# Kernel optimization log

Measured on AMD Instinct MI355X. Metric: run time of the kernel, lower is better.

## Reference

```python
import jax, jax.numpy as jnp
import numpy as np

D = 256        # n_unit
H = 2          # n_head
FF = 256       # n_hid
WIN = 99       # N-1 in source: row i attends to cols [i-99, i]
NEG = -1e30    # additive mask value (-inf in torch)
LN_EPS = 1e-5


def _layer_norm(x, w, b):
    mu = jnp.mean(x, axis=-1, keepdims=True)
    var = jnp.mean((x - mu) ** 2, axis=-1, keepdims=True)
    return (x - mu) * jax.lax.rsqrt(var + LN_EPS) * w + b


def _pos_encoding(S, d):
    pos = jnp.arange(S, dtype=jnp.float32)[:, None]                      # [S,1]
    div = jnp.exp(jnp.arange(0, d, 2, dtype=jnp.float32) * (-np.log(10000.0) / d))
    ang = pos * div                                                      # [S,d/2]
    return jnp.stack([jnp.sin(ang), jnp.cos(ang)], axis=-1).reshape(S, d)


def _band_mask(S):
    i = jnp.arange(S)[:, None]
    j = jnp.arange(S)[None, :]
    allowed = (j <= i) & (j >= i - WIN)
    return jnp.where(allowed, 0.0, NEG).astype(jnp.float32)             # [S,S]


def setup_inputs() -> dict:
    key = jax.random.key(0)
    ks = jax.random.split(key, 24)
    B, S, IN = 8, 2000, 256
    s = 0.02
    inp = {
        "src": jax.random.normal(ks[0], (B, S, IN), jnp.float32),
        "input_lengths": jax.random.randint(ks[1], (B,), 1, S + 1).astype(jnp.int64),
        # encoder Linear(in_size, n_unit); torch Linear weight is [out,in]
        "W_enc": jax.random.normal(ks[2], (D, IN), jnp.float32) * s,
        "b_enc": jnp.zeros((D,), jnp.float32),
        # MHA packed qkv projection
        "in_proj_w": jax.random.normal(ks[3], (3 * D, D), jnp.float32) * s,
        "in_proj_b": jnp.zeros((3 * D,), jnp.float32),
        "out_proj_w": jax.random.normal(ks[4], (D, D), jnp.float32) * s,
        "out_proj_b": jnp.zeros((D,), jnp.float32),
        "ln1_w": jnp.ones((D,), jnp.float32),
        "ln1_b": jnp.zeros((D,), jnp.float32),
        # FFN
        "lin1_w": jax.random.normal(ks[5], (FF, D), jnp.float32) * s,
        "lin1_b": jnp.zeros((FF,), jnp.float32),
        "lin2_w": jax.random.normal(ks[6], (D, FF), jnp.float32) * s,
        "lin2_b": jnp.zeros((D,), jnp.float32),
        "ln2_w": jnp.ones((D,), jnp.float32),
        "ln2_b": jnp.zeros((D,), jnp.float32),
        # output head
        "fc1_w": jax.random.normal(ks[7], (D // 4, D), jnp.float32) * s,
        "fc1_b": jnp.zeros((D // 4,), jnp.float32),
        "fc2_w": jax.random.normal(ks[8], (1, D // 4), jnp.float32) * s,
        "fc2_b": jnp.zeros((1,), jnp.float32),
    }
    return inp


def reference(src, input_lengths, W_enc, b_enc, in_proj_w, in_proj_b,
              out_proj_w, out_proj_b, ln1_w, ln1_b, lin1_w, lin1_b,
              lin2_w, lin2_b, ln2_w, ln2_b, fc1_w, fc1_b, fc2_w, fc2_b):
    B, S, _ = src.shape
    hd = D // H
    # input projection + positional encoding (dropout is identity at eval)
    x = src @ W_enc.T + b_enc                                            # [B,S,D]
    x = x + _pos_encoding(S, D)[None]
    # --- TransformerEncoderLayer (post-norm, relu) with banded causal mask ---
    qkv = x @ in_proj_w.T + in_proj_b                                    # [B,S,3D]
    q, k, v = jnp.split(qkv, 3, axis=-1)
    q = q.reshape(B, S, H, hd)
    k = k.reshape(B, S, H, hd)
    v = v.reshape(B, S, H, hd)
    scores = jnp.einsum('bihd,bjhd->bhij', q, k) / np.sqrt(hd)           # [B,H,S,S]
    scores = scores + _band_mask(S)[None, None]
    attn = jax.nn.softmax(scores, axis=-1)
    ctx = jnp.einsum('bhij,bjhd->bihd', attn, v).reshape(B, S, D)
    attn_out = ctx @ out_proj_w.T + out_proj_b
    x = _layer_norm(x + attn_out, ln1_w, ln1_b)
    ff = jax.nn.relu(x @ lin1_w.T + lin1_b) @ lin2_w.T + lin2_b
    x = _layer_norm(x + ff, ln2_w, ln2_b)
    # --- output head (no activation between fc1 and fc2, per source) ---
    out = x @ fc1_w.T + fc1_b                                            # [B,S,D/4]
    logits = out @ fc2_w.T + fc2_b                                       # [B,S,1]
    return logits.reshape(B, -1)                                         # [B,S]
```

## Files before the change

kernel.cpp:

```cpp
#include <hip/hip_runtime.h>
#include <math.h>

#define SLEN 2000
#define BATCH 8
#define MTOK 16000
#define WIN 99

typedef __attribute__((ext_vector_type(8))) short short8;
typedef __attribute__((ext_vector_type(4))) float floatx4;

__device__ __forceinline__ float bf2f(unsigned int h) {
  union { unsigned int u; float f; } w; w.u = h << 16; return w.f;
}
__device__ __forceinline__ unsigned short f2bf(float f) {
  union { float f; unsigned int u; } w; w.f = f;
  return (unsigned short)((w.u + 0x7fffu + ((w.u >> 16) & 1u)) >> 16);
}

typedef const __attribute__((address_space(1))) unsigned int* gas_t;
typedef __attribute__((address_space(3))) unsigned int* las_t;
__device__ __forceinline__ void gload_lds16(const unsigned short* g, unsigned short* l) {
  __builtin_amdgcn_global_load_lds((gas_t)g, (las_t)l, 16, 0, 0);
}

__device__ __forceinline__ void cvt4(const float* __restrict__ in,
                                     unsigned short* __restrict__ out, int i) {
  float4 v = ((const float4*)in)[i];
  ushort4 o;
  o.x = f2bf(v.x); o.y = f2bf(v.y); o.z = f2bf(v.z); o.w = f2bf(v.w);
  ((ushort4*)out)[i] = o;
}

__global__ __launch_bounds__(256) void k_prep(
    const float* __restrict__ wenc,     unsigned short* __restrict__ wencb,
    const float* __restrict__ wqk,      unsigned short* __restrict__ wqkb,
    const float* __restrict__ wout,     unsigned short* __restrict__ woutb,
    const float* __restrict__ wl1,      unsigned short* __restrict__ wl1b,
    const float* __restrict__ wl2,      unsigned short* __restrict__ wl2b,
    float* __restrict__ pe,
    const float* __restrict__ fc1w, const float* __restrict__ fc1b,
    const float* __restrict__ fc2w, const float* __restrict__ fc2b,
    const float* __restrict__ ln2w, const float* __restrict__ ln2b,
    float* __restrict__ hp) {
  __shared__ float red0[4], red1[4];
  const int bx = blockIdx.x, tid = threadIdx.x;
  if (bx < 64)         { cvt4(wenc, wencb, bx * 256 + tid); }
  else if (bx < 256)   { cvt4(wqk,  wqkb,  (bx - 64) * 256 + tid); }
  else if (bx < 320)   { cvt4(wout, woutb, (bx - 256) * 256 + tid); }
  else if (bx < 384)   { cvt4(wl1,  wl1b,  (bx - 320) * 256 + tid); }
  else if (bx < 448)   { cvt4(wl2,  wl2b,  (bx - 384) * 256 + tid); }
  else if (bx < 2448) {
    int idx = (bx - 448) * 256 + tid;
    int s = idx >> 8, d = idx & 255, p2 = d >> 1;
    float dv  = expf((float)p2 * -0.07195578415606394f);
    float ang = (float)s * dv;
    pe[idx] = (d & 1) ? cosf(ang) : sinf(ang);
  } else {
    int k = tid;
    float we = 0.f;
#pragma unroll 8
    for (int o = 0; o < 64; ++o) we += fc2w[o] * fc1w[o * 256 + k];
    float c1 = ln2w[k] * we;
    hp[k] = c1;
    float p0 = ln2b[k] * we;
    if (k < 64) p0 += fc2w[k] * fc1b[k];
    float s0 = p0, s1 = c1;
#pragma unroll
    for (int off = 32; off; off >>= 1) {
      s0 += __shfl_xor(s0, off);
      s1 += __shfl_xor(s1, off);
    }
    int wv = k >> 6;
    if ((k & 63) == 0) { red0[wv] = s0; red1[wv] = s1; }
    __syncthreads();
    if (k == 0) {
      hp[256] = red0[0] + red0[1] + red0[2] + red0[3] + fc2b[0];
      hp[257] = red1[0] + red1[1] + red1[2] + red1[3];
    }
  }
}

#define XPAD 264

__global__ __launch_bounds__(256) void k_pre(
    const float* __restrict__ src,
    const unsigned short* __restrict__ wenc, const float* __restrict__ benc,
    const float* __restrict__ pe,
    const unsigned short* __restrict__ wqk, const float* __restrict__ bqk,
    unsigned short* __restrict__ xb, unsigned short* __restrict__ qkvb) {
  __shared__ __align__(16) unsigned short Xt[64 * XPAD];
  __shared__ __align__(16) unsigned short Achk[64 * 32];
  __shared__ __align__(16) unsigned short Bchk[256 * 32];
  const int tid = threadIdx.x, lane = tid & 63, w = tid >> 6;
  const int m0 = blockIdx.x * 64;
  const int kq = lane >> 4, ml = lane & 15;
  const int myrow = w * 16 + ml;
  const int cq = lane >> 4, cl = lane & 15;

  const int ar = tid >> 2, as = tid & 3;
  const int ac = as ^ ((ar >> 1) & 3);
  const float* asrc = src + (size_t)(m0 + ar) * 256 + ac * 8;

  int brow[4], bsc[4];
#pragma unroll
  for (int i = 0; i < 4; ++i) {
    brow[i] = (w * 4 + i) * 16 + (lane >> 2);
    bsc[i]  = (lane & 3) ^ ((brow[i] >> 1) & 3);
  }

  floatx4 acc[16] = {};
  for (int kt = 0; kt < 256; kt += 32) {
    __syncthreads();
    {
      float4 v0 = *(const float4*)(asrc + kt);
      float4 v1 = *(const float4*)(asrc + kt + 4);
      unsigned short t8[8] = {f2bf(v0.x), f2bf(v0.y), f2bf(v0.z), f2bf(v0.w),
                              f2bf(v1.x), f2bf(v1.y), f2bf(v1.z), f2bf(v1.w)};
      *(uint4*)&Achk[ar * 32 + as * 8] = *(const uint4*)t8;
    }
#pragma unroll
    for (int i = 0; i < 4; ++i)
      gload_lds16(wenc + (size_t)brow[i] * 256 + kt + bsc[i] * 8, &Bchk[(w * 4 + i) * 512]);
    __syncthreads();

    int sa = kq ^ ((myrow >> 1) & 3);
    short8 af = *(const short8*)&Achk[myrow * 32 + sa * 8];
#pragma unroll
    for (int nt = 0; nt < 16; ++nt) {
      int n = nt * 16 + ml;
      int sb = kq ^ ((n >> 1) & 3);
      short8 bf = *(const short8*)&Bchk[n * 32 + sb * 8];
      acc[nt] = __builtin_amdgcn_mfma_f32_16x16x32_bf16(af, bf, acc[nt], 0, 0, 0);
    }
  }
#pragma unroll
  for (int nt = 0; nt < 16; ++nt) {
#pragma unroll
    for (int r = 0; r < 4; ++r) {
      int lrow = w * 16 + cq * 4 + r;
      int row  = m0 + lrow;
      int col  = nt * 16 + cl;
      float v = acc[nt][r] + benc[col] + pe[(size_t)(row % SLEN) * 256 + col];
      unsigned short hv = f2bf(v);
      Xt[lrow * XPAD + col] = hv;
      xb[(size_t)row * 256 + col] = hv;
    }
  }

  for (int p = 0; p < 3; ++p) {
    floatx4 a2[16] = {};
    for (int kt = 0; kt < 256; kt += 32) {
      __syncthreads();
#pragma unroll
      for (int i = 0; i < 4; ++i)
        gload_lds16(wqk + (size_t)(p * 256 + brow[i]) * 256 + kt + bsc[i] * 8,
                    &Bchk[(w * 4 + i) * 512]);
      __syncthreads();
      short8 af = *(const short8*)&Xt[myrow * XPAD + kt + kq * 8];
#pragma unroll
      for (int nt = 0; nt < 16; ++nt) {
        int n = nt * 16 + ml;
        int sb = kq ^ ((n >> 1) & 3);
        short8 bf = *(const short8*)&Bchk[n * 32 + sb * 8];
        a2[nt] = __builtin_amdgcn_mfma_f32_16x16x32_bf16(af, bf, a2[nt], 0, 0, 0);
      }
    }
#pragma unroll
    for (int nt = 0; nt < 16; ++nt) {
#pragma unroll
      for (int r = 0; r < 4; ++r) {
        int row = m0 + w * 16 + cq * 4 + r;
        int cg  = p * 256 + nt * 16 + cl;
        qkvb[(size_t)row * 768 + cg] = f2bf(a2[nt][r] + bqk[cg]);
      }
    }
  }
}

#define KPAD 136
#define VPAD 184
#define PPAD 132
#define UNION 176

__global__ __launch_bounds__(256) void k_attn_mfma(const unsigned short* __restrict__ qkv,
                                                   unsigned short* __restrict__ ctx) {
  __shared__ __align__(16) unsigned short KV[UNION * KPAD];
  __shared__ __align__(16) unsigned short Ps[4][16 * PPAD];
  const int tid  = threadIdx.x;
  const int lane = tid & 63;
  const int w    = tid >> 6;
  const int i0   = blockIdx.x * 64;
  const int b    = blockIdx.y;
  const int h    = blockIdx.z;
  const int jmin_u = i0 - WIN;
  const float scale = 0.08838834764831845f;

  const int qrow = i0 + w * 16 + (lane & 15);
  const unsigned short* qptr =
      qkv + (size_t)(b * SLEN + min(qrow, SLEN - 1)) * 768 + h * 128 + (lane >> 4) * 8;
  short8 qf[4];
#pragma unroll
  for (int kc = 0; kc < 4; ++kc) qf[kc] = *(const short8*)(qptr + kc * 32);

  for (int it = 0; it < 11; ++it) {
    int idx = it * 256 + tid;
    int row = idx >> 4;
    int c8  = idx & 15;
    int j = jmin_u + row;
    uint4 v = make_uint4(0u, 0u, 0u, 0u);
    if (j >= 0 && j < SLEN)
      v = *(const uint4*)(qkv + (size_t)(b * SLEN + j) * 768 + 256 + h * 128 + c8 * 8);
    *(uint4*)&KV[row * KPAD + c8 * 8] = v;
  }
  __syncthreads();

  const int koff = w * 16;
  floatx4 sc[8] = {};
#pragma unroll
  for (int kt = 0; kt < 8; ++kt) {
#pragma unroll
    for (int kc = 0; kc < 4; ++kc) {
      short8 kf = *(const short8*)&KV[(koff + kt * 16 + (lane & 15)) * KPAD
                                      + kc * 32 + (lane >> 4) * 8];
      sc[kt] = __builtin_amdgcn_mfma_f32_16x16x32_bf16(qf[kc], kf, sc[kt], 0, 0, 0);
    }
  }

  const int qme = i0 + w * 16 + (lane >> 4) * 4;
  const int jme = jmin_u + koff + (lane & 15);
  float mx[4] = {-1e30f, -1e30f, -1e30f, -1e30f};
#pragma unroll
  for (int kt = 0; kt < 8; ++kt) {
#pragma unroll
    for (int r = 0; r < 4; ++r) {
      int j = jme + kt * 16, q = qme + r;
      bool ok = (j >= 0) && (j >= q - WIN) && (j <= q);
      float s = ok ? sc[kt][r] : -1e30f;
      sc[kt][r] = s;
      mx[r] = fmaxf(mx[r], s);
    }
  }
#pragma unroll
  for (int r = 0; r < 4; ++r)
#pragma unroll
    for (int off = 8; off; off >>= 1) mx[r] = fmaxf(mx[r], __shfl_xor(mx[r], off, 16));

  float sum[4] = {0.f, 0.f, 0.f, 0.f};
#pragma unroll
  for (int kt = 0; kt < 8; ++kt)
#pragma unroll
    for (int r = 0; r < 4; ++r) {
      float e = __expf((sc[kt][r] - mx[r]) * scale);
      sc[kt][r] = e;
      sum[r] += e;
    }
#pragma unroll
  for (int r = 0; r < 4; ++r)
#pragma unroll
    for (int off = 8; off; off >>= 1) sum[r] += __shfl_xor(sum[r], off, 16);
  float rinv[4];
#pragma unroll
  for (int r = 0; r < 4; ++r) rinv[r] = 1.f / sum[r];

  unsigned short* pw = &Ps[w][0];
#pragma unroll
  for (int kt = 0; kt < 8; ++kt)
#pragma unroll
    for (int r = 0; r < 4; ++r)
      pw[((lane >> 4) * 4 + r) * PPAD + kt * 16 + (lane & 15)] = f2bf(sc[kt][r]);
  __syncthreads();

  for (int it = 0; it < 12; ++it) {
    int idx = it * 256 + tid;
    int grp = idx >> 6;
    int key = (grp >> 4) * 64 + (idx & 63);
    int c8  = grp & 15;
    if (key < UNION) {
      int j = jmin_u + key;
      uint4 v = make_uint4(0u, 0u, 0u, 0u);
      if (j >= 0 && j < SLEN)
        v = *(const uint4*)(qkv + (size_t)(b * SLEN + j) * 768 + 512 + h * 128 + c8 * 8);
      unsigned short e[8];
      *(uint4*)e = v;
      int d0 = c8 * 8;
#pragma unroll
      for (int i = 0; i < 8; ++i) KV[(d0 + i) * VPAD + key] = e[i];
    }
  }
  __syncthreads();

  floatx4 ov[8] = {};
#pragma unroll
  for (int kc = 0; kc < 4; ++kc) {
    short8 pf = *(const short8*)&pw[(lane & 15) * PPAD + kc * 32 + (lane >> 4) * 8];
#pragma unroll
    for (int dt = 0; dt < 8; ++dt) {
      short8 vf = *(const short8*)&KV[(dt * 16 + (lane & 15)) * VPAD
                                      + koff + kc * 32 + (lane >> 4) * 8];
      ov[dt] = __builtin_amdgcn_mfma_f32_16x16x32_bf16(pf, vf, ov[dt], 0, 0, 0);
    }
  }

#pragma unroll
  for (int dt = 0; dt < 8; ++dt)
#pragma unroll
    for (int r = 0; r < 4; ++r) {
      int q = qme + r;
      if (q < SLEN)
        ctx[(size_t)(b * SLEN + q) * 256 + h * 128 + dt * 16 + (lane & 15)] =
            f2bf(ov[dt][r] * rinv[r]);
    }
}

__global__ __launch_bounds__(256) void k_post(
    const unsigned short* __restrict__ ctx,
    const unsigned short* __restrict__ wout, const float* __restrict__ bout,
    const unsigned short* __restrict__ xb,
    const float* __restrict__ ln1w, const float* __restrict__ ln1b,
    const unsigned short* __restrict__ w1, const float* __restrict__ b1,
    const unsigned short* __restrict__ w2, const float* __restrict__ b2,
    const float* __restrict__ hp, float* __restrict__ out) {
  __shared__ __align__(16) unsigned short X1[64 * XPAD];
  __shared__ __align__(16) unsigned short Achk[64 * 32];
  __shared__ __align__(16) unsigned short Bchk[256 * 32];
  __shared__ float lnp[512];
  __shared__ float c1s[256];
  const int tid = threadIdx.x, lane = tid & 63, w = tid >> 6;
  const int m0 = blockIdx.x * 64;
  const int kq = lane >> 4, ml = lane & 15;
  const int myrow = w * 16 + ml;
  const int cq = lane >> 4, cl = lane & 15;

  lnp[tid] = ln1w[tid];
  lnp[256 + tid] = ln1b[tid];
  c1s[tid] = hp[tid];
  const float c0 = hp[256], sc1 = hp[257];

  int brow[4], bsc[4];
#pragma unroll
  for (int i = 0; i < 4; ++i) {
    brow[i] = (w * 4 + i) * 16 + (lane >> 2);
    bsc[i]  = (lane & 3) ^ ((brow[i] >> 1) & 3);
  }
  const int arow = w * 16 + (lane >> 2);
  const int asc  = (lane & 3) ^ ((arow >> 1) & 3);
  const unsigned short* actx = ctx + (size_t)(m0 + arow) * 256 + asc * 8;

  floatx4 acc[16] = {};
  for (int kt = 0; kt < 256; kt += 32) {
    __syncthreads();
    gload_lds16(actx + kt, &Achk[w * 512]);
#pragma unroll
    for (int i = 0; i < 4; ++i)
      gload_lds16(wout + (size_t)brow[i] * 256 + kt + bsc[i] * 8, &Bchk[(w * 4 + i) * 512]);
    __syncthreads();
    int sa = kq ^ ((myrow >> 1) & 3);
    short8 af = *(const short8*)&Achk[myrow * 32 + sa * 8];
#pragma unroll
    for (int nt = 0; nt < 16; ++nt) {
      int n = nt * 16 + ml;
      int sb = kq ^ ((n >> 1) & 3);
      short8 bf = *(const short8*)&Bchk[n * 32 + sb * 8];
      acc[nt] = __builtin_amdgcn_mfma_f32_16x16x32_bf16(af, bf, acc[nt], 0, 0, 0);
    }
  }
  float s_[4] = {0.f, 0.f, 0.f, 0.f}, q_[4] = {0.f, 0.f, 0.f, 0.f};
#pragma unroll
  for (int nt = 0; nt < 16; ++nt) {
#pragma unroll
    for (int r = 0; r < 4; ++r) {
      int row = m0 + w * 16 + cq * 4 + r;
      int col = nt * 16 + cl;
      float v = acc[nt][r] + bout[col] + bf2f(xb[(size_t)row * 256 + col]);
      acc[nt][r] = v;
      s_[r] += v;
      q_[r] += v * v;
    }
  }
#pragma unroll
  for (int r = 0; r < 4; ++r)
#pragma unroll
    for (int off = 8; off; off >>= 1) {
      s_[r] += __shfl_xor(s_[r], off, 16);
      q_[r] += __shfl_xor(q_[r], off, 16);
    }
  floatx4 x1sav[16];
#pragma unroll
  for (int r = 0; r < 4; ++r) {
    float mu  = s_[r] * (1.f / 256.f);
    float var = q_[r] * (1.f / 256.f) - mu * mu;
    float rr  = rsqrtf(var + 1e-5f);
    int lrow  = w * 16 + cq * 4 + r;
#pragma unroll
    for (int nt = 0; nt < 16; ++nt) {
      int col = nt * 16 + cl;
      float x1 = (acc[nt][r] - mu) * rr * lnp[col] + lnp[256 + col];
      x1sav[nt][r] = x1;
      X1[lrow * XPAD + col] = f2bf(x1);
    }
  }

#pragma unroll
  for (int nt = 0; nt < 16; ++nt) acc[nt] = (floatx4){0.f, 0.f, 0.f, 0.f};
  for (int kt = 0; kt < 256; kt += 32) {
    __syncthreads();
#pragma unroll
    for (int i = 0; i < 4; ++i)
      gload_lds16(w1 + (size_t)brow[i] * 256 + kt + bsc[i] * 8, &Bchk[(w * 4 + i) * 512]);
    __syncthreads();
    short8 af = *(const short8*)&X1[myrow * XPAD + kt + kq * 8];
#pragma unroll
    for (int nt = 0; nt < 16; ++nt) {
      int n = nt * 16 + ml;
      int sb = kq ^ ((n >> 1) & 3);
      short8 bf = *(const short8*)&Bchk[n * 32 + sb * 8];
      acc[nt] = __builtin_amdgcn_mfma_f32_16x16x32_bf16(af, bf, acc[nt], 0, 0, 0);
    }
  }
  __syncthreads();
#pragma unroll
  for (int nt = 0; nt < 16; ++nt) {
#pragma unroll
    for (int r = 0; r < 4; ++r) {
      int lrow = w * 16 + cq * 4 + r;
      int col  = nt * 16 + cl;
      X1[lrow * XPAD + col] = f2bf(fmaxf(acc[nt][r] + b1[col], 0.f));
    }
  }
  __syncthreads();

#pragma unroll
  for (int nt = 0; nt < 16; ++nt) acc[nt] = (floatx4){0.f, 0.f, 0.f, 0.f};
  for (int kt = 0; kt < 256; kt += 32) {
    __syncthreads();
#pragma unroll
    for (int i = 0; i < 4; ++i)
      gload_lds16(w2 + (size_t)brow[i] * 256 + kt + bsc[i] * 8, &Bchk[(w * 4 + i) * 512]);
    __syncthreads();
    short8 af = *(const short8*)&X1[myrow * XPAD + kt + kq * 8];
#pragma unroll
    for (int nt = 0; nt < 16; ++nt) {
      int n = nt * 16 + ml;
      int sb = kq ^ ((n >> 1) & 3);
      short8 bf = *(const short8*)&Bchk[n * 32 + sb * 8];
      acc[nt] = __builtin_amdgcn_mfma_f32_16x16x32_bf16(af, bf, acc[nt], 0, 0, 0);
    }
  }
  float ss[4] = {0.f, 0.f, 0.f, 0.f}, qq[4] = {0.f, 0.f, 0.f, 0.f}, dd[4] = {0.f, 0.f, 0.f, 0.f};
#pragma unroll
  for (int nt = 0; nt < 16; ++nt) {
#pragma unroll
    for (int r = 0; r < 4; ++r) {
      int col = nt * 16 + cl;
      float v = acc[nt][r] + b2[col] + x1sav[nt][r];
      ss[r] += v;
      qq[r] += v * v;
      dd[r] += v * c1s[col];
    }
  }
#pragma unroll
  for (int r = 0; r < 4; ++r)
#pragma unroll
    for (int off = 8; off; off >>= 1) {
      ss[r] += __shfl_xor(ss[r], off, 16);
      qq[r] += __shfl_xor(qq[r], off, 16);
      dd[r] += __shfl_xor(dd[r], off, 16);
    }
  if (cl == 0) {
#pragma unroll
    for (int r = 0; r < 4; ++r) {
      float mu  = ss[r] * (1.f / 256.f);
      float var = qq[r] * (1.f / 256.f) - mu * mu;
      float rr  = rsqrtf(var + 1e-5f);
      out[m0 + w * 16 + cq * 4 + r] = rr * (dd[r] - mu * sc1) + c0;
    }
  }
}

extern "C" void kernel_launch(void* const* d_in, const int* in_sizes, int n_in,
                              void* d_out, int out_size, void* d_ws, size_t ws_size,
                              hipStream_t stream) {
  const float* src        = (const float*)d_in[0];
  const float* W_enc      = (const float*)d_in[2];
  const float* b_enc      = (const float*)d_in[3];
  const float* in_proj_w  = (const float*)d_in[4];
  const float* in_proj_b  = (const float*)d_in[5];
  const float* out_proj_w = (const float*)d_in[6];
  const float* out_proj_b = (const float*)d_in[7];
  const float* ln1_w      = (const float*)d_in[8];
  const float* ln1_b      = (const float*)d_in[9];
  const float* lin1_w     = (const float*)d_in[10];
  const float* lin1_b     = (const float*)d_in[11];
  const float* lin2_w     = (const float*)d_in[12];
  const float* lin2_b     = (const float*)d_in[13];
  const float* ln2_w      = (const float*)d_in[14];
  const float* ln2_b      = (const float*)d_in[15];
  const float* fc1_w      = (const float*)d_in[16];
  const float* fc1_b      = (const float*)d_in[17];
  const float* fc2_w      = (const float*)d_in[18];
  const float* fc2_b      = (const float*)d_in[19];

  char* p = (char*)d_ws;
  float* pe            = (float*)p;           p += (size_t)SLEN * 256 * 4;
  float* hp            = (float*)p;           p += 2048;
  unsigned short* xb   = (unsigned short*)p;  p += (size_t)MTOK * 256 * 2;
  unsigned short* qkvb = (unsigned short*)p;  p += (size_t)MTOK * 768 * 2;
  unsigned short* ctxb = (unsigned short*)p;  p += (size_t)MTOK * 256 * 2;
  unsigned short* wencb= (unsigned short*)p;  p += 256 * 256 * 2;
  unsigned short* wqkb = (unsigned short*)p;  p += 768 * 256 * 2;
  unsigned short* woutb= (unsigned short*)p;  p += 256 * 256 * 2;
  unsigned short* wl1b = (unsigned short*)p;  p += 256 * 256 * 2;
  unsigned short* wl2b = (unsigned short*)p;  p += 256 * 256 * 2;

  k_prep<<<2449, 256, 0, stream>>>(W_enc, wencb, in_proj_w, wqkb,
                                   out_proj_w, woutb, lin1_w, wl1b, lin2_w, wl2b,
                                   pe, fc1_w, fc1_b, fc2_w, fc2_b, ln2_w, ln2_b, hp);
  k_pre<<<MTOK / 64, 256, 0, stream>>>(src, wencb, b_enc, pe, wqkb, in_proj_b, xb, qkvb);
  k_attn_mfma<<<dim3((SLEN + 63) / 64, BATCH, 2), 256, 0, stream>>>(qkvb, ctxb);
  k_post<<<MTOK / 64, 256, 0, stream>>>(ctxb, woutb, out_proj_b, xb, ln1_w, ln1_b,
                                        wl1b, lin1_b, wl2b, lin2_b, hp, (float*)d_out);
}
```

Measured before the change: 174.4 us.

## Merge pre/attention/post kernels into one cooperative persistent kernel with grid syncs

Replaces the three separate launches (projection, attention, post-FFN) with a single cooperative kernel of 512 blocks that runs each phase and separates them with grid-wide syncs. If the cooperative launch fails, it falls back to three launches of the same kernel. The GEMM phases now use 32-row tiles with a 2x2 wave split and double-buffered weight chunks, so each weight load overlaps the MFMA work of the previous chunk. This removes launch gaps and improves per-block overlap, but it adds grid-sync cost and caps occupancy at two blocks per CU on 512 blocks.

```diff
diff --git a/kernel.cpp b/kernel.cpp
--- a/kernel.cpp
+++ b/kernel.cpp
@@ -1,10 +1,14 @@
 #include <hip/hip_runtime.h>
+#include <hip/hip_cooperative_groups.h>
 #include <math.h>
+
+namespace cg = cooperative_groups;
 
 #define SLEN 2000
 #define BATCH 8
 #define MTOK 16000
 #define WIN 99
+#define XPAD 264
 
 typedef __attribute__((ext_vector_type(8))) short short8;
 typedef __attribute__((ext_vector_type(4))) float floatx4;
@@ -80,399 +84,470 @@
   }
 }
 
-#define XPAD 264
-
-__global__ __launch_bounds__(256) void k_pre(
-    const float* __restrict__ src,
-    const unsigned short* __restrict__ wenc, const float* __restrict__ benc,
-    const float* __restrict__ pe,
-    const unsigned short* __restrict__ wqk, const float* __restrict__ bqk,
-    unsigned short* __restrict__ xb, unsigned short* __restrict__ qkvb) {
-  __shared__ __align__(16) unsigned short Xt[64 * XPAD];
-  __shared__ __align__(16) unsigned short Achk[64 * 32];
-  __shared__ __align__(16) unsigned short Bchk[256 * 32];
-  const int tid = threadIdx.x, lane = tid & 63, w = tid >> 6;
-  const int m0 = blockIdx.x * 64;
-  const int kq = lane >> 4, ml = lane & 15;
-  const int myrow = w * 16 + ml;
-  const int cq = lane >> 4, cl = lane & 15;
-
-  const int ar = tid >> 2, as = tid & 3;
-  const int ac = as ^ ((ar >> 1) & 3);
-  const float* asrc = src + (size_t)(m0 + ar) * 256 + ac * 8;
-
-  int brow[4], bsc[4];
-#pragma unroll
-  for (int i = 0; i < 4; ++i) {
-    brow[i] = (w * 4 + i) * 16 + (lane >> 2);
-    bsc[i]  = (lane & 3) ^ ((brow[i] >> 1) & 3);
-  }
-
-  floatx4 acc[16] = {};
-  for (int kt = 0; kt < 256; kt += 32) {
-    __syncthreads();
-    {
-      float4 v0 = *(const float4*)(asrc + kt);
-      float4 v1 = *(const float4*)(asrc + kt + 4);
-      unsigned short t8[8] = {f2bf(v0.x), f2bf(v0.y), f2bf(v0.z), f2bf(v0.w),
-                              f2bf(v1.x), f2bf(v1.y), f2bf(v1.z), f2bf(v1.w)};
-      *(uint4*)&Achk[ar * 32 + as * 8] = *(const uint4*)t8;
-    }
-#pragma unroll
-    for (int i = 0; i < 4; ++i)
-      gload_lds16(wenc + (size_t)brow[i] * 256 + kt + bsc[i] * 8, &Bchk[(w * 4 + i) * 512]);
-    __syncthreads();
-
-    int sa = kq ^ ((myrow >> 1) & 3);
-    short8 af = *(const short8*)&Achk[myrow * 32 + sa * 8];
-#pragma unroll
-    for (int nt = 0; nt < 16; ++nt) {
-      int n = nt * 16 + ml;
-      int sb = kq ^ ((n >> 1) & 3);
-      short8 bf = *(const short8*)&Bchk[n * 32 + sb * 8];
-      acc[nt] = __builtin_amdgcn_mfma_f32_16x16x32_bf16(af, bf, acc[nt], 0, 0, 0);
-    }
-  }
-#pragma unroll
-  for (int nt = 0; nt < 16; ++nt) {
-#pragma unroll
-    for (int r = 0; r < 4; ++r) {
-      int lrow = w * 16 + cq * 4 + r;
-      int row  = m0 + lrow;
-      int col  = nt * 16 + cl;
-      float v = acc[nt][r] + benc[col] + pe[(size_t)(row % SLEN) * 256 + col];
-      unsigned short hv = f2bf(v);
-      Xt[lrow * XPAD + col] = hv;
-      xb[(size_t)row * 256 + col] = hv;
-    }
-  }
-
-  for (int p = 0; p < 3; ++p) {
-    floatx4 a2[16] = {};
-    for (int kt = 0; kt < 256; kt += 32) {
-      __syncthreads();
-#pragma unroll
-      for (int i = 0; i < 4; ++i)
-        gload_lds16(wqk + (size_t)(p * 256 + brow[i]) * 256 + kt + bsc[i] * 8,
-                    &Bchk[(w * 4 + i) * 512]);
-      __syncthreads();
-      short8 af = *(const short8*)&Xt[myrow * XPAD + kt + kq * 8];
-#pragma unroll
-      for (int nt = 0; nt < 16; ++nt) {
-        int n = nt * 16 + ml;
-        int sb = kq ^ ((n >> 1) & 3);
-        short8 bf = *(const short8*)&Bchk[n * 32 + sb * 8];
-        a2[nt] = __builtin_amdgcn_mfma_f32_16x16x32_bf16(af, bf, a2[nt], 0, 0, 0);
-      }
-    }
-#pragma unroll
-    for (int nt = 0; nt < 16; ++nt) {
-#pragma unroll
-      for (int r = 0; r < 4; ++r) {
-        int row = m0 + w * 16 + cq * 4 + r;
-        int cg  = p * 256 + nt * 16 + cl;
-        qkvb[(size_t)row * 768 + cg] = f2bf(a2[nt][r] + bqk[cg]);
-      }
-    }
-  }
-}
+struct MegaArgs {
+  const float* src;
+  const unsigned short* wenc; const float* benc;
+  const float* pe;
+  const unsigned short* wqk; const float* bqk;
+  unsigned short* xb; unsigned short* qkvb;
+  unsigned short* ctxb;
+  const unsigned short* wout; const float* bout;
+  const float* ln1w; const float* ln1b;
+  const unsigned short* w1; const float* b1;
+  const unsigned short* w2; const float* b2;
+  const float* hp; float* out;
+};
 
 #define KPAD 136
 #define VPAD 184
 #define PPAD 132
 #define UNION 176
-
-__global__ __launch_bounds__(256) void k_attn_mfma(const unsigned short* __restrict__ qkv,
-                                                   unsigned short* __restrict__ ctx) {
-  __shared__ __align__(16) unsigned short KV[UNION * KPAD];
-  __shared__ __align__(16) unsigned short Ps[4][16 * PPAD];
+#define SMEM_BYTES 64768
+
+__global__ __launch_bounds__(256, 2) void k_mega(MegaArgs a, int phase) {
+  __shared__ __align__(16) unsigned char smem[SMEM_BYTES];
   const int tid  = threadIdx.x;
   const int lane = tid & 63;
   const int w    = tid >> 6;
-  const int i0   = blockIdx.x * 64;
-  const int b    = blockIdx.y;
-  const int h    = blockIdx.z;
-  const int jmin_u = i0 - WIN;
-  const float scale = 0.08838834764831845f;
-
-  const int qrow = i0 + w * 16 + (lane & 15);
-  const unsigned short* qptr =
-      qkv + (size_t)(b * SLEN + min(qrow, SLEN - 1)) * 768 + h * 128 + (lane >> 4) * 8;
-  short8 qf[4];
-#pragma unroll
-  for (int kc = 0; kc < 4; ++kc) qf[kc] = *(const short8*)(qptr + kc * 32);
-
-  for (int it = 0; it < 11; ++it) {
-    int idx = it * 256 + tid;
-    int row = idx >> 4;
-    int c8  = idx & 15;
-    int j = jmin_u + row;
-    uint4 v = make_uint4(0u, 0u, 0u, 0u);
-    if (j >= 0 && j < SLEN)
-      v = *(const uint4*)(qkv + (size_t)(b * SLEN + j) * 768 + 256 + h * 128 + c8 * 8);
-    *(uint4*)&KV[row * KPAD + c8 * 8] = v;
+  const int bx   = blockIdx.x;
+  const int kq = lane >> 4, ml = lane & 15;
+
+  if ((phase < 0 || phase == 0) && bx < 500) {
+    const int m0 = bx * 32;
+    unsigned short* Xt   = (unsigned short*)smem;
+    unsigned short* Achk = (unsigned short*)(smem + 16896);
+    unsigned short* Bchk = (unsigned short*)(smem + 20992);
+    const int wrow = (w & 1) * 16;
+    const int c0   = (w >> 1) * 128;
+    const int myrow = wrow + ml;
+    const int sa = kq ^ ((myrow >> 1) & 3);
+
+    const int ar = tid >> 3, sub = tid & 7;
+    const int as16 = sub >> 1, ahalf = sub & 1;
+    const int ac = as16 ^ ((ar >> 1) & 3);
+    const float* asrc = a.src + (size_t)(m0 + ar) * 256 + ac * 8 + ahalf * 4;
+    const int aoff = ar * 32 + as16 * 8 + ahalf * 4;
+
+    int brow[4], bsc[4];
+#pragma unroll
+    for (int i = 0; i < 4; ++i) {
+      brow[i] = (w * 4 + i) * 16 + (lane >> 2);
+      bsc[i]  = (lane & 3) ^ ((brow[i] >> 1) & 3);
+    }
+
+    floatx4 acc[8] = {};
+    {
+      float4 v = *(const float4*)asrc;
+      unsigned short t4[4] = {f2bf(v.x), f2bf(v.y), f2bf(v.z), f2bf(v.w)};
+      *(uint2*)&Achk[aoff] = *(const uint2*)t4;
+#pragma unroll
+      for (int i = 0; i < 4; ++i)
+        gload_lds16(a.wenc + (size_t)brow[i] * 256 + bsc[i] * 8, &Bchk[(w * 4 + i) * 512]);
+    }
+    for (int k8 = 0; k8 < 8; ++k8) {
+      __syncthreads();
+      if (k8 < 7) {
+        int nb = (k8 & 1) ^ 1, kt = (k8 + 1) * 32;
+        float4 v = *(const float4*)(asrc + kt);
+        unsigned short t4[4] = {f2bf(v.x), f2bf(v.y), f2bf(v.z), f2bf(v.w)};
+        *(uint2*)&Achk[nb * 1024 + aoff] = *(const uint2*)t4;
+#pragma unroll
+        for (int i = 0; i < 4; ++i)
+          gload_lds16(a.wenc + (size_t)brow[i] * 256 + kt + bsc[i] * 8,
+                      &Bchk[nb * 8192 + (w * 4 + i) * 512]);
+      }
+      int buf = k8 & 1;
+      short8 af = *(const short8*)&Achk[buf * 1024 + myrow * 32 + sa * 8];
+#pragma unroll
+      for (int nt = 0; nt < 8; ++nt) {
+        int n = c0 + nt * 16 + ml;
+        int sb = kq ^ ((n >> 1) & 3);
+        short8 bf = *(const short8*)&Bchk[buf * 8192 + n * 32 + sb * 8];
+        acc[nt] = __builtin_amdgcn_mfma_f32_16x16x32_bf16(af, bf, acc[nt], 0, 0, 0);
+      }
+    }
+#pragma unroll
+    for (int nt = 0; nt < 8; ++nt)
+#pragma unroll
+      for (int r = 0; r < 4; ++r) {
+        int lr  = wrow + kq * 4 + r;
+        int row = m0 + lr;
+        int col = c0 + nt * 16 + ml;
+        float v = acc[nt][r] + a.benc[col] + a.pe[(size_t)(row % SLEN) * 256 + col];
+        unsigned short hv = f2bf(v);
+        Xt[lr * XPAD + col] = hv;
+        a.xb[(size_t)row * 256 + col] = hv;
+      }
+    __syncthreads();
+
+    for (int p = 0; p < 3; ++p) {
+      const unsigned short* Wp = a.wqk + (size_t)p * 65536;
+      floatx4 a2[8] = {};
+#pragma unroll
+      for (int i = 0; i < 4; ++i)
+        gload_lds16(Wp + (size_t)brow[i] * 256 + bsc[i] * 8, &Bchk[(w * 4 + i) * 512]);
+      for (int k8 = 0; k8 < 8; ++k8) {
+        __syncthreads();
+        if (k8 < 7) {
+          int nb = (k8 & 1) ^ 1, kt = (k8 + 1) * 32;
+#pragma unroll
+          for (int i = 0; i < 4; ++i)
+            gload_lds16(Wp + (size_t)brow[i] * 256 + kt + bsc[i] * 8,
+                        &Bchk[nb * 8192 + (w * 4 + i) * 512]);
+        }
+        int buf = k8 & 1;
+        short8 af = *(const short8*)&Xt[myrow * XPAD + k8 * 32 + kq * 8];
+#pragma unroll
+        for (int nt = 0; nt < 8; ++nt) {
+          int n = c0 + nt * 16 + ml;
+          int sb = kq ^ ((n >> 1) & 3);
+          short8 bf = *(const short8*)&Bchk[buf * 8192 + n * 32 + sb * 8];
+          a2[nt] = __builtin_amdgcn_mfma_f32_16x16x32_bf16(af, bf, a2[nt], 0, 0, 0);
+        }
+      }
+#pragma unroll
+      for (int nt = 0; nt < 8; ++nt)
+#pragma unroll
+        for (int r = 0; r < 4; ++r) {
+          int row = m0 + wrow + kq * 4 + r;
+          int cg2 = p * 256 + c0 + nt * 16 + ml;
+          a.qkvb[(size_t)row * 768 + cg2] = f2bf(a2[nt][r] + a.bqk[cg2]);
+        }
+      if (p < 2) __syncthreads();
+    }
   }
-  __syncthreads();
-
-  const int koff = w * 16;
-  floatx4 sc[8] = {};
-#pragma unroll
-  for (int kt = 0; kt < 8; ++kt) {
-#pragma unroll
-    for (int kc = 0; kc < 4; ++kc) {
-      short8 kf = *(const short8*)&KV[(koff + kt * 16 + (lane & 15)) * KPAD
-                                      + kc * 32 + (lane >> 4) * 8];
-      sc[kt] = __builtin_amdgcn_mfma_f32_16x16x32_bf16(qf[kc], kf, sc[kt], 0, 0, 0);
-    }
-  }
-
-  const int qme = i0 + w * 16 + (lane >> 4) * 4;
-  const int jme = jmin_u + koff + (lane & 15);
-  float mx[4] = {-1e30f, -1e30f, -1e30f, -1e30f};
-#pragma unroll
-  for (int kt = 0; kt < 8; ++kt) {
-#pragma unroll
-    for (int r = 0; r < 4; ++r) {
-      int j = jme + kt * 16, q = qme + r;
-      bool ok = (j >= 0) && (j >= q - WIN) && (j <= q);
-      float s = ok ? sc[kt][r] : -1e30f;
-      sc[kt][r] = s;
-      mx[r] = fmaxf(mx[r], s);
-    }
-  }
-#pragma unroll
-  for (int r = 0; r < 4; ++r)
-#pragma unroll
-    for (int off = 8; off; off >>= 1) mx[r] = fmaxf(mx[r], __shfl_xor(mx[r], off, 16));
-
-  float sum[4] = {0.f, 0.f, 0.f, 0.f};
-#pragma unroll
-  for (int kt = 0; kt < 8; ++kt)
-#pragma unroll
-    for (int r = 0; r < 4; ++r) {
-      float e = __expf((sc[kt][r] - mx[r]) * scale);
-      sc[kt][r] = e;
-      sum[r] += e;
-    }
-#pragma unroll
-  for (int r = 0; r < 4; ++r)
-#pragma unroll
-    for (int off = 8; off; off >>= 1) sum[r] += __shfl_xor(sum[r], off, 16);
-  float rinv[4];
-#pragma unroll
-  for (int r = 0; r < 4; ++r) rinv[r] = 1.f / sum[r];
-
-  unsigned short* pw = &Ps[w][0];
-#pragma unroll
-  for (int kt = 0; kt < 8; ++kt)
-#pragma unroll
-    for (int r = 0; r < 4; ++r)
-      pw[((lane >> 4) * 4 + r) * PPAD + kt * 16 + (lane & 15)] = f2bf(sc[kt][r]);
-  __syncthreads();
-
-  for (int it = 0; it < 12; ++it) {
-    int idx = it * 256 + tid;
-    int grp = idx >> 6;
-    int key = (grp >> 4) * 64 + (idx & 63);
-    int c8  = grp & 15;
-    if (key < UNION) {
-      int j = jmin_u + key;
+  if (phase < 0) cg::this_grid().sync();
+
+  if (phase < 0 || phase == 1) {
+    const int u  = bx;
+    const int i0 = (u & 31) * 64;
+    const int b  = (u >> 5) & 7;
+    const int h  = (u >> 8) & 1;
+    unsigned short* KV = (unsigned short*)smem;
+    unsigned short* Ps = (unsigned short*)(smem + 47872);
+    const int jmin_u = i0 - WIN;
+    const float scale = 0.08838834764831845f;
+
+    const int qrow = i0 + w * 16 + (lane & 15);
+    const unsigned short* qptr =
+        a.qkvb + (size_t)(b * SLEN + min(qrow, SLEN - 1)) * 768 + h * 128 + (lane >> 4) * 8;
+    short8 qf[4];
+#pragma unroll
+    for (int kc = 0; kc < 4; ++kc) qf[kc] = *(const short8*)(qptr + kc * 32);
+
+    for (int it = 0; it < 11; ++it) {
+      int idx = it * 256 + tid;
+      int row = idx >> 4;
+      int c8  = idx & 15;
+      int j = jmin_u + row;
       uint4 v = make_uint4(0u, 0u, 0u, 0u);
       if (j >= 0 && j < SLEN)
-        v = *(const uint4*)(qkv + (size_t)(b * SLEN + j) * 768 + 512 + h * 128 + c8 * 8);
-      unsigned short e[8];
-      *(uint4*)e = v;
-      int d0 = c8 * 8;
-#pragma unroll
-      for (int i = 0; i < 8; ++i) KV[(d0 + i) * VPAD + key] = e[i];
-    }
+        v = *(const uint4*)(a.qkvb + (size_t)(b * SLEN + j) * 768 + 256 + h * 128 + c8 * 8);
+      *(uint4*)&KV[row * KPAD + c8 * 8] = v;
+    }
+    __syncthreads();
+
+    const int koff = w * 16;
+    floatx4 sc[8] = {};
+#pragma unroll
+    for (int kt = 0; kt < 8; ++kt) {
+#pragma unroll
+      for (int kc = 0; kc < 4; ++kc) {
+        short8 kf = *(const short8*)&KV[(koff + kt * 16 + (lane & 15)) * KPAD
+                                        + kc * 32 + (lane >> 4) * 8];
+        sc[kt] = __builtin_amdgcn_mfma_f32_16x16x32_bf16(qf[kc], kf, sc[kt], 0, 0, 0);
+      }
+    }
+
+    const int qme = i0 + w * 16 + (lane >> 4) * 4;
+    const int jme = jmin_u + koff + (lane & 15);
+    float mx[4] = {-1e30f, -1e30f, -1e30f, -1e30f};
+#pragma unroll
+    for (int kt = 0; kt < 8; ++kt) {
+#pragma unroll
+      for (int r = 0; r < 4; ++r) {
+        int j = jme + kt * 16, q = qme + r;
+        bool ok = (j >= 0) && (j >= q - WIN) && (j <= q);
+        float s = ok ? sc[kt][r] : -1e30f;
+        sc[kt][r] = s;
+        mx[r] = fmaxf(mx[r], s);
+      }
+    }
+#pragma unroll
+    for (int r = 0; r < 4; ++r)
+#pragma unroll
+      for (int off = 8; off; off >>= 1) mx[r] = fmaxf(mx[r], __shfl_xor(mx[r], off, 16));
+
+    float sum[4] = {0.f, 0.f, 0.f, 0.f};
+#pragma unroll
+    for (int kt = 0; kt < 8; ++kt)
+#pragma unroll
+      for (int r = 0; r < 4; ++r) {
+        float e = __expf((sc[kt][r] - mx[r]) * scale);
+        sc[kt][r] = e;
+        sum[r] += e;
+      }
+#pragma unroll
+    for (int r = 0; r < 4; ++r)
+#pragma unroll
+      for (int off = 8; off; off >>= 1) sum[r] += __shfl_xor(sum[r], off, 16);
+    float rinv[4];
+#pragma unroll
+    for (int r = 0; r < 4; ++r) rinv[r] = 1.f / sum[r];
+
+    unsigned short* pw = Ps + w * (16 * PPAD);
+#pragma unroll
+    for (int kt = 0; kt < 8; ++kt)
+#pragma unroll
+      for (int r = 0; r < 4; ++r)
+        pw[((lane >> 4) * 4 + r) * PPAD + kt * 16 + (lane & 15)] = f2bf(sc[kt][r]);
+    __syncthreads();
+
+    for (int it = 0; it < 12; ++it) {
+      int idx = it * 256 + tid;
+      int grp = idx >> 6;
+      int key = (grp >> 4) * 64 + (idx & 63);
+      int c8  = grp & 15;
+      if (key < UNION) {
+        int j = jmin_u + key;
+        uint4 v = make_uint4(0u, 0u, 0u, 0u);
+        if (j >= 0 && j < SLEN)
+          v = *(const uint4*)(a.qkvb + (size_t)(b * SLEN + j) * 768 + 512 + h * 128 + c8 * 8);
+        unsigned short e[8];
+        *(uint4*)e = v;
+        int d0 = c8 * 8;
+#pragma unroll
+        for (int i = 0; i < 8; ++i) KV[(d0 + i) * VPAD + key] = e[i];
+      }
+    }
+    __syncthreads();
+
+    floatx4 ov[8] = {};
+#pragma unroll
+    for (int kc = 0; kc < 4; ++kc) {
+      short8 pf = *(const short8*)&pw[(lane & 15) * PPAD + kc * 32 + (lane >> 4) * 8];
+#pragma unroll
+      for (int dt = 0; dt < 8; ++dt) {
+        short8 vf = *(const short8*)&KV[(dt * 16 + (lane & 15)) * VPAD
+                                        + koff + kc * 32 + (lane >> 4) * 8];
+        ov[dt] = __builtin_amdgcn_mfma_f32_16x16x32_bf16(pf, vf, ov[dt], 0, 0, 0);
+      }
+    }
+
+#pragma unroll
+    for (int dt = 0; dt < 8; ++dt)
+#pragma unroll
+      for (int r = 0; r < 4; ++r) {
+        int q = qme + r;
+        if (q < SLEN)
+          a.ctxb[(size_t)(b * SLEN + q) * 256 + h * 128 + dt * 16 + (lane & 15)] =
+              f2bf(ov[dt][r] * rinv[r]);
+      }
   }
-  __syncthreads();
-
-  floatx4 ov[8] = {};
-#pragma unroll
-  for (int kc = 0; kc < 4; ++kc) {
-    short8 pf = *(const short8*)&pw[(lane & 15) * PPAD + kc * 32 + (lane >> 4) * 8];
-#pragma unroll
-    for (int dt = 0; dt < 8; ++dt) {
-      short8 vf = *(const short8*)&KV[(dt * 16 + (lane & 15)) * VPAD
-                                      + koff + kc * 32 + (lane >> 4) * 8];
-      ov[dt] = __builtin_amdgcn_mfma_f32_16x16x32_bf16(pf, vf, ov[dt], 0, 0, 0);
-    }
-  }
-
-#pragma unroll
-  for (int dt = 0; dt < 8; ++dt)
+  if (phase < 0) cg::this_grid().sync();
+
+  if ((phase < 0 || phase == 2) && bx < 500) {
+    const int m0 = bx * 32;
+    unsigned short* X1   = (unsigned short*)smem;
+    unsigned short* Achk = (unsigned short*)(smem + 16896);
+    unsigned short* Bchk = (unsigned short*)(smem + 20992);
+    float* lnred = (float*)(smem + 53760);
+    float* lnp   = (float*)(smem + 54528);
+    float* c1s   = (float*)(smem + 56576);
+    const int wrow = (w & 1) * 16;
+    const int c0   = (w >> 1) * 128;
+    const int half = w >> 1;
+    const int myrow = wrow + ml;
+    const int sa = kq ^ ((myrow >> 1) & 3);
+
+    lnp[tid] = a.ln1w[tid];
+    lnp[256 + tid] = a.ln1b[tid];
+    c1s[tid] = a.hp[tid];
+    const float c0h = a.hp[256], sc1 = a.hp[257];
+
+    int brow[4], bsc[4];
+#pragma unroll
+    for (int i = 0; i < 4; ++i) {
+      brow[i] = (w * 4 + i) * 16 + (lane >> 2);
+      bsc[i]  = (lane & 3) ^ ((brow[i] >> 1) & 3);
+    }
+    const int arow = (w & 1) * 16 + (lane >> 2);
+    const int aasc = (lane & 3) ^ ((arow >> 1) & 3);
+    const unsigned short* actx = a.ctxb + (size_t)(m0 + arow) * 256 + aasc * 8;
+
+    floatx4 acc[8] = {};
+    {
+      if (w < 2) gload_lds16(actx, &Achk[w * 512]);
+#pragma unroll
+      for (int i = 0; i < 4; ++i)
+        gload_lds16(a.wout + (size_t)brow[i] * 256 + bsc[i] * 8, &Bchk[(w * 4 + i) * 512]);
+    }
+    for (int k8 = 0; k8 < 8; ++k8) {
+      __syncthreads();
+      if (k8 < 7) {
+        int nb = (k8 & 1) ^ 1, kt = (k8 + 1) * 32;
+        if (w < 2) gload_lds16(actx + kt, &Achk[nb * 1024 + w * 512]);
+#pragma unroll
+        for (int i = 0; i < 4; ++i)
+          gload_lds16(a.wout + (size_t)brow[i] * 256 + kt + bsc[i] * 8,
+                      &Bchk[nb * 8192 + (w * 4 + i) * 512]);
+      }
+      int buf = k8 & 1;
+      short8 af = *(const short8*)&Achk[buf * 1024 + myrow * 32 + sa * 8];
+#pragma unroll
+      for (int nt = 0; nt < 8; ++nt) {
+        int n = c0 + nt * 16 + ml;
+        int sb = kq ^ ((n >> 1) & 3);
+        short8 bf = *(const short8*)&Bchk[buf * 8192 + n * 32 + sb * 8];
+        acc[nt] = __builtin_amdgcn_mfma_f32_16x16x32_bf16(af, bf, acc[nt], 0, 0, 0);
+      }
+    }
+    float s_[4] = {0.f, 0.f, 0.f, 0.f}, q_[4] = {0.f, 0.f, 0.f, 0.f};
+#pragma unroll
+    for (int nt = 0; nt < 8; ++nt)
+#pragma unroll
+      for (int r = 0; r < 4; ++r) {
+        int row = m0 + wrow + kq * 4 + r;
+        int col = c0 + nt * 16 + ml;
+        float v = acc[nt][r] + a.bout[col] + bf2f(a.xb[(size_t)row * 256 + col]);
+        acc[nt][r] = v;
+        s_[r] += v;
+        q_[r] += v * v;
+      }
+#pragma unroll
+    for (int r = 0; r < 4; ++r)
+#pragma unroll
+      for (int off = 8; off; off >>= 1) {
+        s_[r] += __shfl_xor(s_[r], off, 16);
+        q_[r] += __shfl_xor(q_[r], off, 16);
+      }
+    if (ml == 0) {
+#pragma unroll
+      for (int r = 0; r < 4; ++r) {
+        int lr = wrow + kq * 4 + r;
+        lnred[half * 96 + lr * 3 + 0] = s_[r];
+        lnred[half * 96 + lr * 3 + 1] = q_[r];
+      }
+    }
+    __syncthreads();
+    floatx4 x1sav[8];
 #pragma unroll
     for (int r = 0; r < 4; ++r) {
-      int q = qme + r;
-      if (q < SLEN)
-        ctx[(size_t)(b * SLEN + q) * 256 + h * 128 + dt * 16 + (lane & 15)] =
-            f2bf(ov[dt][r] * rinv[r]);
-    }
-}
-
-__global__ __launch_bounds__(256) void k_post(
-    const unsigned short* __restrict__ ctx,
-    const unsigned short* __restrict__ wout, const float* __restrict__ bout,
-    const unsigned short* __restrict__ xb,
-    const float* __restrict__ ln1w, const float* __restrict__ ln1b,
-    const unsigned short* __restrict__ w1, const float* __restrict__ b1,
-    const unsigned short* __restrict__ w2, const float* __restrict__ b2,
-    const float* __restrict__ hp, float* __restrict__ out) {
-  __shared__ __align__(16) unsigned short X1[64 * XPAD];
-  __shared__ __align__(16) unsigned short Achk[64 * 32];
-  __shared__ __align__(16) unsigned short Bchk[256 * 32];
-  __shared__ float lnp[512];
-  __shared__ float c1s[256];
-  const int tid = threadIdx.x, lane = tid & 63, w = tid >> 6;
-  const int m0 = blockIdx.x * 64;
-  const int kq = lane >> 4, ml = lane & 15;
-  const int myrow = w * 16 + ml;
-  const int cq = lane >> 4, cl = lane & 15;
-
-  lnp[tid] = ln1w[tid];
-  lnp[256 + tid] = ln1b[tid];
-  c1s[tid] = hp[tid];
-  const float c0 = hp[256], sc1 = hp[257];
-
-  int brow[4], bsc[4];
-#pragma unroll
-  for (int i = 0; i < 4; ++i) {
-    brow[i] = (w * 4 + i) * 16 + (lane >> 2);
-    bsc[i]  = (lane & 3) ^ ((brow[i] >> 1) & 3);
-  }
-  const int arow = w * 16 + (lane >> 2);
-  const int asc  = (lane & 3) ^ ((arow >> 1) & 3);
-  const unsigned short* actx = ctx + (size_t)(m0 + arow) * 256 + asc * 8;
-
-  floatx4 acc[16] = {};
-  for (int kt = 0; kt < 256; kt += 32) {
-    __syncthreads();
-    gload_lds16(actx + kt, &Achk[w * 512]);
+      int lr = wrow + kq * 4 + r;
+      float s = lnred[lr * 3 + 0] + lnred[96 + lr * 3 + 0];
+      float q = lnred[lr * 3 + 1] + lnred[96 + lr * 3 + 1];
+      float mu  = s * (1.f / 256.f);
+      float var = q * (1.f / 256.f) - mu * mu;
+      float rr  = rsqrtf(var + 1e-5f);
+#pragma unroll
+      for (int nt = 0; nt < 8; ++nt) {
+        int col = c0 + nt * 16 + ml;
+        float x1 = (acc[nt][r] - mu) * rr * lnp[col] + lnp[256 + col];
+        x1sav[nt][r] = x1;
+        X1[lr * XPAD + col] = f2bf(x1);
+      }
+    }
+    __syncthreads();
+
+#pragma unroll
+    for (int nt = 0; nt < 8; ++nt) acc[nt] = (floatx4){0.f, 0.f, 0.f, 0.f};
 #pragma unroll
     for (int i = 0; i < 4; ++i)
-      gload_lds16(wout + (size_t)brow[i] * 256 + kt + bsc[i] * 8, &Bchk[(w * 4 + i) * 512]);
-    __syncthreads();
-    int sa = kq ^ ((myrow >> 1) & 3);
-    short8 af = *(const short8*)&Achk[myrow * 32 + sa * 8];
-#pragma unroll
-    for (int nt = 0; nt < 16; ++nt) {
-      int n = nt * 16 + ml;
-      int sb = kq ^ ((n >> 1) & 3);
-      short8 bf = *(const short8*)&Bchk[n * 32 + sb * 8];
-      acc[nt] = __builtin_amdgcn_mfma_f32_16x16x32_bf16(af, bf, acc[nt], 0, 0, 0);
-    }
-  }
-  float s_[4] = {0.f, 0.f, 0.f, 0.f}, q_[4] = {0.f, 0.f, 0.f, 0.f};
-#pragma unroll
-  for (int nt = 0; nt < 16; ++nt) {
-#pragma unroll
-    for (int r = 0; r < 4; ++r) {
-      int row = m0 + w * 16 + cq * 4 + r;
-      int col = nt * 16 + cl;
-      float v = acc[nt][r] + bout[col] + bf2f(xb[(size_t)row * 256 + col]);
-      acc[nt][r] = v;
-      s_[r] += v;
-      q_[r] += v * v;
-    }
-  }
-#pragma unroll
-  for (int r = 0; r < 4; ++r)
-#pragma unroll
-    for (int off = 8; off; off >>= 1) {
-      s_[r] += __shfl_xor(s_[r], off, 16);
-      q_[r] += __shfl_xor(q_[r], off, 16);
-    }
-  floatx4 x1sav[16];
-#pragma unroll
-  for (int r = 0; r < 4; ++r) {
-    float mu  = s_[r] * (1.f / 256.f);
-    float var = q_[r] * (1.f / 256.f) - mu * mu;
-    float rr  = rsqrtf(var + 1e-5f);
-    int lrow  = w * 16 + cq * 4 + r;
-#pragma unroll
-    for (int nt = 0; nt < 16; ++nt) {
-      int col = nt * 16 + cl;
-      float x1 = (acc[nt][r] - mu) * rr * lnp[col] + lnp[256 + col];
-      x1sav[nt][r] = x1;
-      X1[lrow * XPAD + col] = f2bf(x1);
-    }
-  }
-
-#pragma unroll
-  for (int nt = 0; nt < 16; ++nt) acc[nt] = (floatx4){0.f, 0.f, 0.f, 0.f};
-  for (int kt = 0; kt < 256; kt += 32) {
-    __syncthreads();
+      gload_lds16(a.w1 + (size_t)brow[i] * 256 + bsc[i] * 8, &Bchk[(w * 4 + i) * 512]);
+    for (int k8 = 0; k8 < 8; ++k8) {
+      __syncthreads();
+      if (k8 < 7) {
+        int nb = (k8 & 1) ^ 1, kt = (k8 + 1) * 32;
+#pragma unroll
+        for (int i = 0; i < 4; ++i)
+          gload_lds16(a.w1 + (size_t)brow[i] * 256 + kt + bsc[i] * 8,
+                      &Bchk[nb * 8192 + (w * 4 + i) * 512]);
+      }
+      int buf = k8 & 1;
+      short8 af = *(const short8*)&X1[myrow * XPAD + k8 * 32 + kq * 8];
+#pragma unroll
+      for (int nt = 0; nt < 8; ++nt) {
+        int n = c0 + nt * 16 + ml;
+        int sb = kq ^ ((n >> 1) & 3);
+        short8 bf = *(const short8*)&Bchk[buf * 8192 + n * 32 + sb * 8];
+        acc[nt] = __builtin_amdgcn_mfma_f32_16x16x32_bf16(af, bf, acc[nt], 0, 0, 0);
+      }
+    }
+    __syncthreads();
+#pragma unroll
+    for (int nt = 0; nt < 8; ++nt)
+#pragma unroll
+      for (int r = 0; r < 4; ++r) {
+        int lr  = wrow + kq * 4 + r;
+        int col = c0 + nt * 16 + ml;
+        X1[lr * XPAD + col] = f2bf(fmaxf(acc[nt][r] + a.b1[col], 0.f));
+      }
+
+#pragma unroll
+    for (int nt = 0; nt < 8; ++nt) acc[nt] = (floatx4){0.f, 0.f, 0.f, 0.f};
 #pragma unroll
     for (int i = 0; i < 4; ++i)
-      gload_lds16(w1 + (size_t)brow[i] * 256 + kt + bsc[i] * 8, &Bchk[(w * 4 + i) * 512]);
-    __syncthreads();
-    short8 af = *(const short8*)&X1[myrow * XPAD + kt + kq * 8];
-#pragma unroll
-    for (int nt = 0; nt < 16; ++nt) {
-      int n = nt * 16 + ml;
-      int sb = kq ^ ((n >> 1) & 3);
-      short8 bf = *(const short8*)&Bchk[n * 32 + sb * 8];
-      acc[nt] = __builtin_amdgcn_mfma_f32_16x16x32_bf16(af, bf, acc[nt], 0, 0, 0);
-    }
-  }
-  __syncthreads();
-#pragma unroll
-  for (int nt = 0; nt < 16; ++nt) {
-#pragma unroll
-    for (int r = 0; r < 4; ++r) {
-      int lrow = w * 16 + cq * 4 + r;
-      int col  = nt * 16 + cl;
-      X1[lrow * XPAD + col] = f2bf(fmaxf(acc[nt][r] + b1[col], 0.f));
-    }
-  }
-  __syncthreads();
-
-#pragma unroll
-  for (int nt = 0; nt < 16; ++nt) acc[nt] = (floatx4){0.f, 0.f, 0.f, 0.f};
-  for (int kt = 0; kt < 256; kt += 32) {
-    __syncthreads();
-#pragma unroll
-    for (int i = 0; i < 4; ++i)
-      gload_lds16(w2 + (size_t)brow[i] * 256 + kt + bsc[i] * 8, &Bchk[(w * 4 + i) * 512]);
-    __syncthreads();
-    short8 af = *(const short8*)&X1[myrow * XPAD + kt + kq * 8];
-#pragma unroll
-    for (int nt = 0; nt < 16; ++nt) {
-      int n = nt * 16 + ml;
-      int sb = kq ^ ((n >> 1) & 3);
-      short8 bf = *(const short8*)&Bchk[n * 32 + sb * 8];
-      acc[nt] = __builtin_amdgcn_mfma_f32_16x16x32_bf16(af, bf, acc[nt], 0, 0, 0);
-    }
-  }
-  float ss[4] = {0.f, 0.f, 0.f, 0.f}, qq[4] = {0.f, 0.f, 0.f, 0.f}, dd[4] = {0.f, 0.f, 0.f, 0.f};
-#pragma unroll
-  for (int nt = 0; nt < 16; ++nt) {
-#pragma unroll
-    for (int r = 0; r < 4; ++r) {
-      int col = nt * 16 + cl;
-      float v = acc[nt][r] + b2[col] + x1sav[nt][r];
-      ss[r] += v;
-      qq[r] += v * v;
-      dd[r] += v * c1s[col];
-    }
-  }
-#pragma unroll
-  for (int r = 0; r < 4; ++r)
-#pragma unroll
-    for (int off = 8; off; off >>= 1) {
-      ss[r] += __shfl_xor(ss[r], off, 16);
-      qq[r] += __shfl_xor(qq[r], off, 16);
-      dd[r] += __shfl_xor(dd[r], off, 16);
-    }
-  if (cl == 0) {
-#pragma unroll
-    for (int r = 0; r < 4; ++r) {
-      float mu  = ss[r] * (1.f / 256.f);
-      float var = qq[r] * (1.f / 256.f) - mu * mu;
-      float rr  = rsqrtf(var + 1e-5f);
-      out[m0 + w * 16 + cq * 4 + r] = rr * (dd[r] - mu * sc1) + c0;
+      gload_lds16(a.w2 + (size_t)brow[i] * 256 + bsc[i] * 8, &Bchk[(w * 4 + i) * 512]);
+    for (int k8 = 0; k8 < 8; ++k8) {
+      __syncthreads();
+      if (k8 < 7) {
+        int nb = (k8 & 1) ^ 1, kt = (k8 + 1) * 32;
+#pragma unroll
+        for (int i = 0; i < 4; ++i)
+          gload_lds16(a.w2 + (size_t)brow[i] * 256 + kt + bsc[i] * 8,
+                      &Bchk[nb * 8192 + (w * 4 + i) * 512]);
+      }
+      int buf = k8 & 1;
+      short8 af = *(const short8*)&X1[myrow * XPAD + k8 * 32 + kq * 8];
+#pragma unroll
+      for (int nt = 0; nt < 8; ++nt) {
+        int n = c0 + nt * 16 + ml;
+        int sb = kq ^ ((n >> 1) & 3);
+        short8 bf = *(const short8*)&Bchk[buf * 8192 + n * 32 + sb * 8];
+        acc[nt] = __builtin_amdgcn_mfma_f32_16x16x32_bf16(af, bf, acc[nt], 0, 0, 0);
+      }
+    }
+    float ss[4] = {0.f, 0.f, 0.f, 0.f}, qq[4] = {0.f, 0.f, 0.f, 0.f}, dd[4] = {0.f, 0.f, 0.f, 0.f};
+#pragma unroll
+    for (int nt = 0; nt < 8; ++nt)
+#pragma unroll
+      for (int r = 0; r < 4; ++r) {
+        int col = c0 + nt * 16 + ml;
+        float v = acc[nt][r] + a.b2[col] + x1sav[nt][r];
+        ss[r] += v;
+        qq[r] += v * v;
+        dd[r] += v * c1s[col];
+      }
+#pragma unroll
+    for (int r = 0; r < 4; ++r)
+#pragma unroll
+      for (int off = 8; off; off >>= 1) {
+        ss[r] += __shfl_xor(ss[r], off, 16);
+        qq[r] += __shfl_xor(qq[r], off, 16);
+        dd[r] += __shfl_xor(dd[r], off, 16);
+      }
+    if (ml == 0) {
+#pragma unroll
+      for (int r = 0; r < 4; ++r) {
+        int lr = wrow + kq * 4 + r;
+        lnred[half * 96 + lr * 3 + 0] = ss[r];
+        lnred[half * 96 + lr * 3 + 1] = qq[r];
+        lnred[half * 96 + lr * 3 + 2] = dd[r];
+      }
+    }
+    __syncthreads();
+    if (w < 2 && ml == 0) {
+#pragma unroll
+      for (int r = 0; r < 4; ++r) {
+        int lr = wrow + kq * 4 + r;
+        float s = lnred[lr * 3 + 0] + lnred[96 + lr * 3 + 0];
+        float q = lnred[lr * 3 + 1] + lnred[96 + lr * 3 + 1];
+        float d = lnred[lr * 3 + 2] + lnred[96 + lr * 3 + 2];
+        float mu  = s * (1.f / 256.f);
+        float var = q * (1.f / 256.f) - mu * mu;
+        float rr  = rsqrtf(var + 1e-5f);
+        a.out[m0 + lr] = rr * (d - mu * sc1) + c0h;
+      }
     }
   }
 }
@@ -515,8 +590,24 @@
   k_prep<<<2449, 256, 0, stream>>>(W_enc, wencb, in_proj_w, wqkb,
                                    out_proj_w, woutb, lin1_w, wl1b, lin2_w, wl2b,
                                    pe, fc1_w, fc1_b, fc2_w, fc2_b, ln2_w, ln2_b, hp);
-  k_pre<<<MTOK / 64, 256, 0, stream>>>(src, wencb, b_enc, pe, wqkb, in_proj_b, xb, qkvb);
-  k_attn_mfma<<<dim3((SLEN + 63) / 64, BATCH, 2), 256, 0, stream>>>(qkvb, ctxb);
-  k_post<<<MTOK / 64, 256, 0, stream>>>(ctxb, woutb, out_proj_b, xb, ln1_w, ln1_b,
-                                        wl1b, lin1_b, wl2b, lin2_b, hp, (float*)d_out);
+
+  MegaArgs ma;
+  ma.src = src;  ma.wenc = wencb; ma.benc = b_enc; ma.pe = pe;
+  ma.wqk = wqkb; ma.bqk = in_proj_b;
+  ma.xb = xb; ma.qkvb = qkvb; ma.ctxb = ctxb;
+  ma.wout = woutb; ma.bout = out_proj_b;
+  ma.ln1w = ln1_w; ma.ln1b = ln1_b;
+  ma.w1 = wl1b; ma.b1 = lin1_b;
+  ma.w2 = wl2b; ma.b2 = lin2_b;
+  ma.hp = hp; ma.out = (float*)d_out;
+
+  int ph = -1;
+  void* kargs[] = { (void*)&ma, (void*)&ph };
+  hipError_t e = hipLaunchCooperativeKernel((const void*)k_mega, dim3(512), dim3(256),
+                                            kargs, 0, stream);
+  if (e != hipSuccess) {
+    k_mega<<<512, 256, 0, stream>>>(ma, 0);
+    k_mega<<<512, 256, 0, stream>>>(ma, 1);
+    k_mega<<<512, 256, 0, stream>>>(ma, 2);
+  }
 }
```

Measured after the change: 323.3 us. +85.4%, slower.
